# Kernel tuning notes

Measured on AMD Instinct MI355X. Metric: run time of the kernel, lower is better.

Reference implementation:

```python
import jax, jax.numpy as jnp
import numpy as np

B, H, W = 4, 256, 256
DIM, DIM_OUT, NUM_HEADS = 96, 192, 3
WS = 8            # window_size
QS = 2            # q_stride (2,2)
HIDDEN = int(DIM_OUT * 4.0)
EPS = 1e-6


def layernorm(x, g, b):
    m = jnp.mean(x, axis=-1, keepdims=True)
    v = jnp.mean(jnp.square(x - m), axis=-1, keepdims=True)
    return (x - m) * jax.lax.rsqrt(v + EPS) * g + b


def maxpool2x2(x):
    # x: [..., h, w, c] -> [..., h//2, w//2, c]
    s = x.shape
    x = x.reshape(s[:-3] + (s[-3] // QS, QS, s[-2] // QS, QS, s[-1]))
    return x.max(axis=(-4, -2))


def setup_inputs() -> dict:
    key = jax.random.key(0)
    ks = jax.random.split(key, 16)
    std = 0.02
    return {
        "x": jax.random.normal(ks[0], (B, H, W, DIM), dtype=jnp.float32),
        "norm1_g": jnp.ones((DIM,), jnp.float32),
        "norm1_b": jnp.zeros((DIM,), jnp.float32),
        "proj_w": jax.random.normal(ks[1], (DIM, DIM_OUT), jnp.float32) * std,
        "proj_b": jnp.zeros((DIM_OUT,), jnp.float32),
        "qkv_w": jax.random.normal(ks[2], (DIM, 3 * DIM_OUT), jnp.float32) * std,
        "qkv_b": jnp.zeros((3 * DIM_OUT,), jnp.float32),
        "attn_proj_w": jax.random.normal(ks[3], (DIM_OUT, DIM_OUT), jnp.float32) * std,
        "attn_proj_b": jnp.zeros((DIM_OUT,), jnp.float32),
        "norm2_g": jnp.ones((DIM_OUT,), jnp.float32),
        "norm2_b": jnp.zeros((DIM_OUT,), jnp.float32),
        "mlp_w1": jax.random.normal(ks[4], (DIM_OUT, HIDDEN), jnp.float32) * std,
        "mlp_b1": jnp.zeros((HIDDEN,), jnp.float32),
        "mlp_w2": jax.random.normal(ks[5], (HIDDEN, DIM_OUT), jnp.float32) * std,
        "mlp_b2": jnpp_zeros if False else jnp.zeros((DIM_OUT,), jnp.float32),
    }


def reference(x, norm1_g, norm1_b, proj_w, proj_b, qkv_w, qkv_b,
              attn_proj_w, attn_proj_b, norm2_g, norm2_b,
              mlp_w1, mlp_b1, mlp_w2, mlp_b2):
    b, h, w, _ = x.shape
    xn = layernorm(x, norm1_g, norm1_b)

    # dim != dim_out: shortcut = proj(norm(x)), then pooled by q_stride
    shortcut = xn @ proj_w + proj_b                       # [B,H,W,Do]
    shortcut = maxpool2x2(shortcut)                       # [B,H/2,W/2,Do]

    # window partition (H,W divisible by WS -> no padding)
    nh, nw = h // WS, w // WS
    xw = xn.reshape(b, nh, WS, nw, WS, DIM).transpose(0, 1, 3, 2, 4, 5)
    xw = xw.reshape(b * nh * nw, WS, WS, DIM)             # [Bw,WS,WS,C]
    Bw = xw.shape[0]

    # MultiScaleAttention with q pooling
    hd = DIM_OUT // NUM_HEADS
    qkv = (xw @ qkv_w + qkv_b).reshape(Bw, WS * WS, 3, NUM_HEADS, hd)
    q, k, v = qkv[:, :, 0], qkv[:, :, 1], qkv[:, :, 2]    # [Bw,N,h,d]
    q = maxpool2x2(q.reshape(Bw, WS, WS, DIM_OUT))        # [Bw,WS/2,WS/2,Do]
    wq = WS // QS
    q = q.reshape(Bw, wq * wq, NUM_HEADS, hd)

    scale = 1.0 / jnp.sqrt(jnp.asarray(hd, x.dtype))
    scores = jnp.einsum('bqhd,bkhd->bhqk', q, k) * scale
    probs = jax.nn.softmax(scores, axis=-1)
    out = jnp.einsum('bhqk,bkhd->bqhd', probs, v).reshape(Bw, wq, wq, DIM_OUT)
    out = out @ attn_proj_w + attn_proj_b                 # [Bw,wq,wq,Do]

    # window unpartition at pooled resolution
    hp, wp = h // QS, w // QS
    out = out.reshape(b, nh, nw, wq, wq, DIM_OUT).transpose(0, 1, 3, 2, 4, 5)
    out = out.reshape(b, hp, wp, DIM_OUT)

    y = shortcut + out
    yn = layernorm(y, norm2_g, norm2_b)
    mlp = jax.nn.gelu(yn @ mlp_w1 + mlp_b1, approximate=False) @ mlp_w2 + mlp_b2
    return y + mlp
```

## Files before the change

### kernel.cpp

```cpp
#include <hip/hip_runtime.h>
#include <hip/hip_bf16.h>
#include <math.h>

#define EPSV 1e-6f

typedef __attribute__((ext_vector_type(8))) short bf16x8;
typedef __attribute__((ext_vector_type(4))) float f32x4;
typedef __attribute__((ext_vector_type(4))) unsigned short u16x4;

__device__ inline float bf2f(unsigned short u) {
  union { unsigned int i; float f; } v;
  v.i = ((unsigned int)u) << 16;
  return v.f;
}
__device__ inline unsigned short f2bf(float f) {
  unsigned int u = __builtin_bit_cast(unsigned int, f);
  u += 0x7FFFu + ((u >> 16) & 1u);
  return (unsigned short)(u >> 16);
}
__device__ inline float fast_gelu(float v) {
  float u = 1.5957691216057308f * (v + 0.044715f * v * v * v);
  float t = __expf(-u);
  return v * __builtin_amdgcn_rcpf(1.f + t);
}

__global__ __launch_bounds__(256) void k0_pack(
    const float* __restrict__ qw, const float* __restrict__ aw,
    const float* __restrict__ w1, const float* __restrict__ w2,
    const float* __restrict__ pw, unsigned short* __restrict__ qwp,
    unsigned short* __restrict__ awp, unsigned short* __restrict__ w1p,
    unsigned short* __restrict__ w2p, unsigned short* __restrict__ pwp) {
  int idx = blockIdx.x * 256 + threadIdx.x;
  int lane = idx & 63;
  int l15 = lane & 15, quad = lane >> 4;
  if (idx < 6912) {
    int fi = idx >> 6;
    int ntile = fi / 3, kstep = fi - ntile * 3;
    int n = ntile * 16 + l15, k0 = kstep * 32 + quad * 8;
#pragma unroll
    for (int j = 0; j < 8; ++j)
      qwp[(size_t)idx * 8 + j] = f2bf(qw[(size_t)(k0 + j) * 576 + n]);
  } else if (idx < 11520) {
    int i2 = idx - 6912;
    int fi = i2 >> 6;
    int ntile = fi / 6, kstep = fi - ntile * 6;
    int n = ntile * 16 + l15, k0 = kstep * 32 + quad * 8;
#pragma unroll
    for (int j = 0; j < 8; ++j)
      awp[(size_t)i2 * 8 + j] = f2bf(aw[(size_t)(k0 + j) * 192 + n]);
  } else if (idx < 29952) {
    int i3 = idx - 11520;
    int fi = i3 >> 6;
    int ntile = fi / 6, kstep = fi - ntile * 6;
    int n = ntile * 16 + l15, k0 = kstep * 32 + quad * 8;
#pragma unroll
    for (int j = 0; j < 8; ++j)
      w1p[(size_t)i3 * 8 + j] = f2bf(w1[(size_t)(k0 + j) * 768 + n]);
  } else if (idx < 48384) {
    int i4 = idx - 29952;
    int fi = i4 >> 6;
    int ntile = fi / 24, kstep = fi - ntile * 24;
    int n = ntile * 16 + l15, k0 = kstep * 32 + quad * 8;
#pragma unroll
    for (int j = 0; j < 8; ++j)
      w2p[(size_t)i4 * 8 + j] = f2bf(w2[(size_t)(k0 + j) * 192 + n]);
  } else if (idx < 50688) {
    int i5 = idx - 48384;
    int fi = i5 >> 6;
    int ntile = fi / 3, kstep = fi - ntile * 3;
    int n = ntile * 16 + l15, k0 = kstep * 32 + quad * 8;
#pragma unroll
    for (int j = 0; j < 8; ++j)
      pwp[(size_t)i5 * 8 + j] = f2bf(pw[(size_t)(k0 + j) * 192 + n]);
  }
}

__global__ __launch_bounds__(256) void k1234_fused(
    const float* __restrict__ x, const float* __restrict__ n1g,
    const float* __restrict__ n1b, const unsigned short* __restrict__ pwp,
    const float* __restrict__ pb, const unsigned short* __restrict__ qwp,
    const float* __restrict__ qb, const unsigned short* __restrict__ awp,
    const float* __restrict__ ab, const float* __restrict__ n2g,
    const float* __restrict__ n2b, const unsigned short* __restrict__ w1p,
    const float* __restrict__ b1, const unsigned short* __restrict__ w2p,
    const float* __restrict__ b2, float* __restrict__ out) {
  __shared__ __align__(16) unsigned char smem[72960];
  unsigned short (*kk)[200] = (unsigned short (*)[200])smem;
  unsigned short (*vT)[72] = (unsigned short (*)[72])(smem + 25600);
  unsigned short (*wbuf)[16][72] =
      (unsigned short (*)[16][72])(smem + 53248);
  float (*sc)[200] = (float (*)[200])(smem + 60160);
  unsigned short (*yn)[196] = (unsigned short (*)[196])(smem + 25600);
  unsigned short (*hls)[196] = (unsigned short (*)[196])(smem + 25600 + 6272);

  int tid = threadIdx.x, wave = tid >> 6, lane = tid & 63;
  int wi = blockIdx.x;
  int b = wi >> 10, nh = (wi >> 5) & 31, nw = wi & 31;
  int grow0 = nh * 8, gcol0 = nw * 8;
  int l15 = lane & 15, quad = lane >> 4;

  {
    int tt = tid >> 2, sub = tid & 3;
    int rr = tt >> 3, cc = tt & 7;
    size_t tok = (size_t)((b * 256 + grow0 + rr) * 256 + gcol0 + cc);
    const f32x4* xr4 = (const f32x4*)(x + tok * 96 + sub * 24);
    f32x4 v[6];
#pragma unroll
    for (int i = 0; i < 6; ++i) v[i] = xr4[i];
    float s = 0.f;
#pragma unroll
    for (int i = 0; i < 6; ++i)
#pragma unroll
      for (int j = 0; j < 4; ++j) s += v[i][j];
    s += __shfl_xor(s, 1);
    s += __shfl_xor(s, 2);
    float mean = s * (1.f / 96.f);
    float q = 0.f;
#pragma unroll
    for (int i = 0; i < 6; ++i)
#pragma unroll
      for (int j = 0; j < 4; ++j) {
        float d = v[i][j] - mean;
        q += d * d;
      }
    q += __shfl_xor(q, 1);
    q += __shfl_xor(q, 2);
    float rstd = rsqrtf(q * (1.f / 96.f) + EPSV);
    const f32x4* g4 = (const f32x4*)(n1g + sub * 24);
    const f32x4* b4 = (const f32x4*)(n1b + sub * 24);
#pragma unroll
    for (int i = 0; i < 6; ++i) {
      f32x4 gg = g4[i], bb = b4[i];
      u16x4 o;
#pragma unroll
      for (int j = 0; j < 4; ++j)
        o[j] = f2bf((v[i][j] - mean) * rstd * gg[j] + bb[j]);
      *(u16x4*)(&kk[tt][sub * 24 + i * 4]) = o;
    }
  }
  __syncthreads();

  bf16x8 areg[4][3];
#pragma unroll
  for (int mt = 0; mt < 4; ++mt)
#pragma unroll
    for (int ks = 0; ks < 3; ++ks)
      areg[mt][ks] = *(const bf16x8*)(&kk[mt * 16 + l15][ks * 32 + quad * 8]);
  __syncthreads();

#pragma unroll
  for (int nl = 0; nl < 3; ++nl) {
    int nt = wave * 3 + nl;
    const unsigned short* bp = pwp + ((size_t)(nt * 3) * 64 + lane) * 8;
    bf16x8 b0 = *(const bf16x8*)(bp);
    bf16x8 b1v = *(const bf16x8*)(bp + 512);
    bf16x8 b2v = *(const bf16x8*)(bp + 1024);
    int c = nt * 16 + l15;
    float bias = pb[c];
#pragma unroll
    for (int mt = 0; mt < 4; ++mt) {
      f32x4 acc = {0.f, 0.f, 0.f, 0.f};
      acc = __builtin_amdgcn_mfma_f32_16x16x32_bf16(areg[mt][0], b0, acc, 0, 0, 0);
      acc = __builtin_amdgcn_mfma_f32_16x16x32_bf16(areg[mt][1], b1v, acc, 0, 0, 0);
      acc = __builtin_amdgcn_mfma_f32_16x16x32_bf16(areg[mt][2], b2v, acc, 0, 0, 0);
      float p0 = fmaxf(acc[0], acc[1]);
      float p1 = fmaxf(acc[2], acc[3]);
      float q0 = fmaxf(p0, __shfl_xor(p0, 32));
      float q1 = fmaxf(p1, __shfl_xor(p1, 32));
      if (quad < 2) {
        int p = mt * 4 + quad * 2;
        sc[p][c] = q0 + bias;
        sc[p + 1][c] = q1 + bias;
      }
    }
  }

#pragma unroll
  for (int aj = 0; aj < 9; ++aj) {
    int type, hh, nt;
    if (wave < 3) {
      if (aj < 4) { type = 0; hh = wave; nt = aj; }
      else { int kv = wave * 5 + (aj - 4); type = 1 + kv / 12; int t2 = kv % 12; hh = t2 >> 2; nt = t2 & 3; }
    } else {
      int kv = 15 + aj; type = 1 + kv / 12; int t2 = kv % 12; hh = t2 >> 2; nt = t2 & 3;
    }
    int gnt = type * 12 + hh * 4 + nt;
    const unsigned short* bp = qwp + (size_t)gnt * 1536 + lane * 8;
    bf16x8 b0 = *(const bf16x8*)(bp);
    bf16x8 b1v = *(const bf16x8*)(bp + 512);
    bf16x8 b2v = *(const bf16x8*)(bp + 1024);
    int dloc = nt * 16 + l15;
    int dglob = hh * 64 + dloc;
    float bias = qb[type * 192 + dglob];
#pragma unroll
    for (int mt = 0; mt < 4; ++mt) {
      f32x4 acc = {0.f, 0.f, 0.f, 0.f};
      acc = __builtin_amdgcn_mfma_f32_16x16x32_bf16(areg[mt][0], b0, acc, 0, 0, 0);
      acc = __builtin_amdgcn_mfma_f32_16x16x32_bf16(areg[mt][1], b1v, acc, 0, 0, 0);
      acc = __builtin_amdgcn_mfma_f32_16x16x32_bf16(areg[mt][2], b2v, acc, 0, 0, 0);
      if (type == 0) {
        float p0 = fmaxf(acc[0], acc[1]);
        float p1 = fmaxf(acc[2], acc[3]);
        float q0 = fmaxf(p0, __shfl_xor(p0, 32));
        float q1 = fmaxf(p1, __shfl_xor(p1, 32));
        if (quad < 2) {
          int p = mt * 4 + quad * 2;
          wbuf[wave][p][dloc] = f2bf(q0 + bias);
          wbuf[wave][p + 1][dloc] = f2bf(q1 + bias);
        }
      } else if (type == 1) {
        int t0 = mt * 16 + quad * 4;
#pragma unroll
        for (int r = 0; r < 4; ++r) kk[t0 + r][dglob] = f2bf(acc[r] + bias);
      } else {
        int t0 = mt * 16 + quad * 4;
        u16x4 pk;
#pragma unroll
        for (int r = 0; r < 4; ++r) pk[r] = f2bf(acc[r] + bias);
        *(u16x4*)(&vT[dglob][t0]) = pk;
      }
    }
  }
  __syncthreads();

  f32x4 o4[4];
  if (wave < 3) {
    int h = wave;
    bf16x8 aq0 = *(const bf16x8*)(&wbuf[wave][l15][quad * 8]);
    bf16x8 aq1 = *(const bf16x8*)(&wbuf[wave][l15][32 + quad * 8]);
    f32x4 s4[4];
#pragma unroll
    for (int kt = 0; kt < 4; ++kt) {
      bf16x8 bk0 = *(const bf16x8*)(&kk[kt * 16 + l15][h * 64 + quad * 8]);
      bf16x8 bk1 = *(const bf16x8*)(&kk[kt * 16 + l15][h * 64 + 32 + quad * 8]);
      f32x4 s = {0.f, 0.f, 0.f, 0.f};
      s = __builtin_amdgcn_mfma_f32_16x16x32_bf16(aq0, bk0, s, 0, 0, 0);
      s = __builtin_amdgcn_mfma_f32_16x16x32_bf16(aq1, bk1, s, 0, 0, 0);
      s4[kt] = s;
    }
    float ps[4][4];
#pragma unroll
    for (int r = 0; r < 4; ++r) {
      float m = fmaxf(fmaxf(s4[0][r], s4[1][r]), fmaxf(s4[2][r], s4[3][r]));
#pragma unroll
      for (int o = 8; o; o >>= 1) m = fmaxf(m, __shfl_xor(m, o));
      float sm = 0.f;
#pragma unroll
      for (int kt = 0; kt < 4; ++kt) {
        float e = __expf((s4[kt][r] - m) * 0.125f);
        ps[kt][r] = e;
        sm += e;
      }
#pragma unroll
      for (int o = 8; o; o >>= 1) sm += __shfl_xor(sm, o);
      float inv = __builtin_amdgcn_rcpf(sm);
#pragma unroll
      for (int kt = 0; kt < 4; ++kt) ps[kt][r] *= inv;
    }
#pragma unroll
    for (int kt = 0; kt < 4; ++kt)
#pragma unroll
      for (int r = 0; r < 4; ++r)
        wbuf[wave][quad * 4 + r][kt * 16 + l15] = f2bf(ps[kt][r]);
    bf16x8 ap0 = *(const bf16x8*)(&wbuf[wave][l15][quad * 8]);
    bf16x8 ap1 = *(const bf16x8*)(&wbuf[wave][l15][32 + quad * 8]);
#pragma unroll
    for (int dt = 0; dt < 4; ++dt) {
      bf16x8 bv0 = *(const bf16x8*)(&vT[h * 64 + dt * 16 + l15][quad * 8]);
      bf16x8 bv1 = *(const bf16x8*)(&vT[h * 64 + dt * 16 + l15][32 + quad * 8]);
      f32x4 o = {0.f, 0.f, 0.f, 0.f};
      o = __builtin_amdgcn_mfma_f32_16x16x32_bf16(ap0, bv0, o, 0, 0, 0);
      o = __builtin_amdgcn_mfma_f32_16x16x32_bf16(ap1, bv1, o, 0, 0, 0);
      o4[dt] = o;
    }
  }
  __syncthreads();

  if (wave < 3) {
    int h = wave;
#pragma unroll
    for (int dt = 0; dt < 4; ++dt)
#pragma unroll
      for (int r = 0; r < 4; ++r)
        kk[quad * 4 + r][h * 64 + dt * 16 + l15] = f2bf(o4[dt][r]);
  }
  __syncthreads();

  bf16x8 ao[6];
#pragma unroll
  for (int ks = 0; ks < 6; ++ks)
    ao[ks] = *(const bf16x8*)(&kk[l15][ks * 32 + quad * 8]);
#pragma unroll
  for (int nl = 0; nl < 3; ++nl) {
    int ntl = wave * 3 + nl;
    const unsigned short* bp = awp + (size_t)ntl * 3072 + lane * 8;
    f32x4 acc = {0.f, 0.f, 0.f, 0.f};
#pragma unroll
    for (int ks = 0; ks < 6; ++ks) {
      bf16x8 bw = *(const bf16x8*)(bp + ks * 512);
      acc = __builtin_amdgcn_mfma_f32_16x16x32_bf16(ao[ks], bw, acc, 0, 0, 0);
    }
    int cc = ntl * 16 + l15;
    float bias = ab[cc];
#pragma unroll
    for (int r = 0; r < 4; ++r) {
      int p = quad * 4 + r;
      sc[p][cc] += acc[r] + bias;
    }
  }
  __syncthreads();

  {
    int tt = wave * 4 + quad;
    const f32x4* y4 = (const f32x4*)(&sc[tt][l15 * 12]);
    f32x4 vv[3];
    vv[0] = y4[0]; vv[1] = y4[1]; vv[2] = y4[2];
    float s = 0.f;
#pragma unroll
    for (int i = 0; i < 3; ++i)
#pragma unroll
      for (int j = 0; j < 4; ++j) s += vv[i][j];
    s += __shfl_xor(s, 1);
    s += __shfl_xor(s, 2);
    s += __shfl_xor(s, 4);
    s += __shfl_xor(s, 8);
    float mean = s * (1.f / 192.f);
    float q = 0.f;
#pragma unroll
    for (int i = 0; i < 3; ++i)
#pragma unroll
      for (int j = 0; j < 4; ++j) {
        float d = vv[i][j] - mean;
        q += d * d;
      }
    q += __shfl_xor(q, 1);
    q += __shfl_xor(q, 2);
    q += __shfl_xor(q, 4);
    q += __shfl_xor(q, 8);
    float rstd = rsqrtf(q * (1.f / 192.f) + EPSV);
    const f32x4* g4 = (const f32x4*)(n2g + l15 * 12);
    const f32x4* b4 = (const f32x4*)(n2b + l15 * 12);
#pragma unroll
    for (int i = 0; i < 3; ++i) {
      f32x4 gg = g4[i], bb = b4[i];
      u16x4 o;
#pragma unroll
      for (int j = 0; j < 4; ++j)
        o[j] = f2bf((vv[i][j] - mean) * rstd * gg[j] + bb[j]);
      *(u16x4*)(&yn[tt][l15 * 12 + i * 4]) = o;
    }
  }
  __syncthreads();

  bf16x8 ar[6];
#pragma unroll
  for (int ks = 0; ks < 6; ++ks)
    ar[ks] = *(const bf16x8*)(&yn[l15][ks * 32 + quad * 8]);

  f32x4 acc2[3];
#pragma unroll
  for (int nl = 0; nl < 3; ++nl) acc2[nl] = (f32x4){0.f, 0.f, 0.f, 0.f};

  for (int c = 0; c < 4; ++c) {
#pragma unroll
    for (int nl = 0; nl < 3; ++nl) {
      int gnt = c * 12 + wave * 3 + nl;
      const unsigned short* bp = w1p + ((size_t)(gnt * 6) * 64 + lane) * 8;
      f32x4 t0 = {0.f, 0.f, 0.f, 0.f};
#pragma unroll
      for (int ks = 0; ks < 6; ++ks) {
        bf16x8 bw = *(const bf16x8*)(bp + ks * 512);
        t0 = __builtin_amdgcn_mfma_f32_16x16x32_bf16(ar[ks], bw, t0, 0, 0, 0);
      }
      int lcol = wave * 48 + nl * 16 + l15;
      float bias = b1[c * 192 + lcol];
#pragma unroll
      for (int r = 0; r < 4; ++r)
        hls[quad * 4 + r][lcol] = f2bf(fast_gelu(t0[r] + bias));
    }
    __syncthreads();
    bf16x8 hr[6];
#pragma unroll
    for (int ks = 0; ks < 6; ++ks)
      hr[ks] = *(const bf16x8*)(&hls[l15][ks * 32 + quad * 8]);
#pragma unroll
    for (int nl = 0; nl < 3; ++nl) {
      int nt2 = wave * 3 + nl;
      const unsigned short* bp =
          w2p + ((size_t)(nt2 * 24 + c * 6) * 64 + lane) * 8;
#pragma unroll
      for (int ks = 0; ks < 6; ++ks) {
        bf16x8 bw = *(const bf16x8*)(bp + ks * 512);
        acc2[nl] =
            __builtin_amdgcn_mfma_f32_16x16x32_bf16(hr[ks], bw, acc2[nl], 0, 0, 0);
      }
    }
    __syncthreads();
  }

#pragma unroll
  for (int nl = 0; nl < 3; ++nl) {
    int col = (wave * 3 + nl) * 16 + l15;
    float bias = b2[col];
#pragma unroll
    for (int r = 0; r < 4; ++r) {
      int p = quad * 4 + r;
      int hp = nh * 4 + (p >> 2), wp2 = nw * 4 + (p & 3);
      size_t oi = ((size_t)((b * 128 + hp) * 128 + wp2)) * 192 + col;
      out[oi] = sc[p][col] + acc2[nl][r] + bias;
    }
  }
}

extern "C" void kernel_launch(void* const* d_in, const int* in_sizes, int n_in,
                              void* d_out, int out_size, void* d_ws,
                              size_t ws_size, hipStream_t stream) {
  const float* x = (const float*)d_in[0];
  const float* n1g = (const float*)d_in[1];
  const float* n1b = (const float*)d_in[2];
  const float* pw = (const float*)d_in[3];
  const float* pb = (const float*)d_in[4];
  const float* qw = (const float*)d_in[5];
  const float* qb = (const float*)d_in[6];
  const float* aw = (const float*)d_in[7];
  const float* ab = (const float*)d_in[8];
  const float* n2g = (const float*)d_in[9];
  const float* n2b = (const float*)d_in[10];
  const float* w1 = (const float*)d_in[11];
  const float* b1 = (const float*)d_in[12];
  const float* w2 = (const float*)d_in[13];
  const float* b2 = (const float*)d_in[14];
  float* out = (float*)d_out;

  char* wsb = (char*)d_ws;
  unsigned short* qwp = (unsigned short*)wsb;
  unsigned short* awp = (unsigned short*)(wsb + 110592);
  unsigned short* w1p = (unsigned short*)(wsb + 184320);
  unsigned short* w2p = (unsigned short*)(wsb + 479232);
  unsigned short* pwp = (unsigned short*)(wsb + 774144);

  hipLaunchKernelGGL(k0_pack, dim3(198), dim3(256), 0, stream, qw, aw, w1, w2,
                     pw, qwp, awp, w1p, w2p, pwp);
  hipLaunchKernelGGL(k1234_fused, dim3(4096), dim3(256), 0, stream, x, n1g,
                     n1b, pwp, pb, qwp, qb, awp, ab, n2g, n2b, w1p, b1, w2p,
                     b2, out);
}
```

Measured before the change: 361.5 us.

## Alias K and V^T in shared memory by computing V after scores

Restructures the fused window-attention kernel so the V projection is computed only after the QK^T scores have been read out of shared memory, letting V^T reuse the K buffer. The yn/hls/sc buffers are repacked, cutting LDS from about 73KB to about 47KB per block so more blocks can be resident per CU. The cost is an extra __syncthreads and serialising the V projection after the score MFMAs. The score registers are also kept live across that phase, which adds register pressure.

```diff
diff --git a/kernel.cpp b/kernel.cpp
--- a/kernel.cpp
+++ b/kernel.cpp
@@ -84,14 +84,14 @@
     const float* __restrict__ n2b, const unsigned short* __restrict__ w1p,
     const float* __restrict__ b1, const unsigned short* __restrict__ w2p,
     const float* __restrict__ b2, float* __restrict__ out) {
-  __shared__ __align__(16) unsigned char smem[72960];
+  __shared__ __align__(16) unsigned char smem[46848];
   unsigned short (*kk)[200] = (unsigned short (*)[200])smem;
-  unsigned short (*vT)[72] = (unsigned short (*)[72])(smem + 25600);
+  unsigned short (*vT)[72] = (unsigned short (*)[72])smem;
   unsigned short (*wbuf)[16][72] =
-      (unsigned short (*)[16][72])(smem + 53248);
-  float (*sc)[200] = (float (*)[200])(smem + 60160);
-  unsigned short (*yn)[196] = (unsigned short (*)[196])(smem + 25600);
-  unsigned short (*hls)[196] = (unsigned short (*)[196])(smem + 25600 + 6272);
+      (unsigned short (*)[16][72])(smem + 27648);
+  float (*sc)[192] = (float (*)[192])(smem + 34560);
+  unsigned short (*yn)[200] = (unsigned short (*)[200])(smem + 6400);
+  unsigned short (*hls)[200] = (unsigned short (*)[200])(smem + 12800);
 
   int tid = threadIdx.x, wave = tid >> 6, lane = tid & 63;
   int wi = blockIdx.x;
@@ -176,13 +176,13 @@
   }
 
 #pragma unroll
-  for (int aj = 0; aj < 9; ++aj) {
+  for (int aj = 0; aj < 6; ++aj) {
     int type, hh, nt;
     if (wave < 3) {
       if (aj < 4) { type = 0; hh = wave; nt = aj; }
-      else { int kv = wave * 5 + (aj - 4); type = 1 + kv / 12; int t2 = kv % 12; hh = t2 >> 2; nt = t2 & 3; }
+      else { int kidx = wave * 2 + (aj - 4); type = 1; hh = kidx >> 2; nt = kidx & 3; }
     } else {
-      int kv = 15 + aj; type = 1 + kv / 12; int t2 = kv % 12; hh = t2 >> 2; nt = t2 & 3;
+      int kidx = 6 + aj; type = 1; hh = kidx >> 2; nt = kidx & 3;
     }
     int gnt = type * 12 + hh * 4 + nt;
     const unsigned short* bp = qwp + (size_t)gnt * 1536 + lane * 8;
@@ -208,27 +208,20 @@
           wbuf[wave][p][dloc] = f2bf(q0 + bias);
           wbuf[wave][p + 1][dloc] = f2bf(q1 + bias);
         }
-      } else if (type == 1) {
-        int t0 = mt * 16 + quad * 4;
-#pragma unroll
-        for (int r = 0; r < 4; ++r) kk[t0 + r][dglob] = f2bf(acc[r] + bias);
       } else {
         int t0 = mt * 16 + quad * 4;
-        u16x4 pk;
-#pragma unroll
-        for (int r = 0; r < 4; ++r) pk[r] = f2bf(acc[r] + bias);
-        *(u16x4*)(&vT[dglob][t0]) = pk;
-      }
-    }
-  }
-  __syncthreads();
-
-  f32x4 o4[4];
+#pragma unroll
+        for (int r = 0; r < 4; ++r) kk[t0 + r][dglob] = f2bf(acc[r] + bias);
+      }
+    }
+  }
+  __syncthreads();
+
+  f32x4 s4[4];
   if (wave < 3) {
     int h = wave;
     bf16x8 aq0 = *(const bf16x8*)(&wbuf[wave][l15][quad * 8]);
     bf16x8 aq1 = *(const bf16x8*)(&wbuf[wave][l15][32 + quad * 8]);
-    f32x4 s4[4];
 #pragma unroll
     for (int kt = 0; kt < 4; ++kt) {
       bf16x8 bk0 = *(const bf16x8*)(&kk[kt * 16 + l15][h * 64 + quad * 8]);
@@ -238,6 +231,35 @@
       s = __builtin_amdgcn_mfma_f32_16x16x32_bf16(aq1, bk1, s, 0, 0, 0);
       s4[kt] = s;
     }
+  }
+  __syncthreads();
+
+#pragma unroll
+  for (int vj = 0; vj < 3; ++vj) {
+    int vidx = wave * 3 + vj;
+    int hh = vidx >> 2, nt = vidx & 3;
+    const unsigned short* bp =
+        qwp + (size_t)(24 + hh * 4 + nt) * 1536 + lane * 8;
+    bf16x8 b0 = *(const bf16x8*)(bp);
+    bf16x8 b1v = *(const bf16x8*)(bp + 512);
+    bf16x8 b2v = *(const bf16x8*)(bp + 1024);
+    int dglob = hh * 64 + nt * 16 + l15;
+    float bias = qb[384 + dglob];
+#pragma unroll
+    for (int mt = 0; mt < 4; ++mt) {
+      f32x4 acc = {0.f, 0.f, 0.f, 0.f};
+      acc = __builtin_amdgcn_mfma_f32_16x16x32_bf16(areg[mt][0], b0, acc, 0, 0, 0);
+      acc = __builtin_amdgcn_mfma_f32_16x16x32_bf16(areg[mt][1], b1v, acc, 0, 0, 0);
+      acc = __builtin_amdgcn_mfma_f32_16x16x32_bf16(areg[mt][2], b2v, acc, 0, 0, 0);
+      int t0 = mt * 16 + quad * 4;
+      u16x4 pk;
+#pragma unroll
+      for (int r = 0; r < 4; ++r) pk[r] = f2bf(acc[r] + bias);
+      *(u16x4*)(&vT[dglob][t0]) = pk;
+    }
+  }
+
+  if (wave < 3) {
     float ps[4][4];
 #pragma unroll
     for (int r = 0; r < 4; ++r) {
@@ -262,6 +284,12 @@
 #pragma unroll
       for (int r = 0; r < 4; ++r)
         wbuf[wave][quad * 4 + r][kt * 16 + l15] = f2bf(ps[kt][r]);
+  }
+  __syncthreads();
+
+  f32x4 o4[4];
+  if (wave < 3) {
+    int h = wave;
     bf16x8 ap0 = *(const bf16x8*)(&wbuf[wave][l15][quad * 8]);
     bf16x8 ap1 = *(const bf16x8*)(&wbuf[wave][l15][32 + quad * 8]);
 #pragma unroll
```

After: 317.8 us. 12.1% less time.
